# Kernel optimization log

Measured on AMD Instinct MI355X. Metric: run time of the kernel, lower is better.

The kernel has to match this reference:

```python
import jax, jax.numpy as jnp
import numpy as np

K, D = 512, 256
NUM_CLASSES, SHARED_KEYS = 10, 10
B, H, W = 32, 64, 64
TRAINING = True


def setup_inputs() -> dict:
    key = jax.random.key(0)
    k1, k2, k3 = jax.random.split(key, 3)
    z_e_x = jax.random.normal(k1, (B, D, H, W), dtype=jnp.float32)
    labels = jax.random.randint(k2, (B,), 0, NUM_CLASSES)
    # nn.Embedding weight initialized uniform(-1/K, 1/K)
    codebook = jax.random.uniform(k3, (K, D), minval=-1.0 / K, maxval=1.0 / K,
                                  dtype=jnp.float32)
    return {"z_e_x": z_e_x, "codebook": codebook, "labels": labels}


def _irrelevant_regions(labels_flat, k, num_classes, n_shared, training):
    # uniform partition of the first K - n_shared codes over the classes
    uniform = jnp.round(jnp.linspace(-0.5, num_classes - 0.51, k - n_shared))  # [K-Ns]
    irrel = uniform[None, :] != labels_flat[:, None].astype(uniform.dtype)     # [N, K-Ns]
    n = labels_flat.shape[0]
    if training:
        tail = jnp.ones((n, n_shared), dtype=bool)   # TRAIN: shared keys masked out
    else:
        tail = jnp.zeros((n, n_shared), dtype=bool)
    return jnp.concatenate([irrel, tail], axis=1)    # [N, K]


def reference(z_e_x, codebook, labels):
    x = jnp.transpose(z_e_x, (0, 2, 3, 1))           # [B,H,W,D]
    xf = x.reshape(-1, D)                            # [N,D], N=B*H*W
    labels_flat = jnp.repeat(labels, H * W)          # [N]

    irrel = _irrelevant_regions(labels_flat, K, NUM_CLASSES, SHARED_KEYS, TRAINING)

    cb_sqr = jnp.sum(codebook * codebook, axis=1)                      # [K]
    in_sqr = jnp.sum(xf * xf, axis=1, keepdims=True)                   # [N,1]
    distances = in_sqr + cb_sqr[None, :] - 2.0 * (xf @ codebook.T)     # [N,K]
    distances = jnp.where(irrel, jnp.inf, distances)

    idx = jnp.argmin(distances, axis=1)                                # [N]

    codes = codebook[idx].reshape(x.shape)                             # [B,H,W,D]
    # straight-through path (detached codebook in torch)
    z_q = x + jax.lax.stop_gradient(codes - x)
    z_q_x = jnp.transpose(z_q, (0, 3, 1, 2))                           # [B,D,H,W]
    # non-detached codebook lookup path
    z_q_bar = codebook[jax.lax.stop_gradient(idx)].reshape(x.shape)
    z_q_x_bar = jnp.transpose(z_q_bar, (0, 3, 1, 2))                   # [B,D,H,W]
    return (z_q_x, z_q_x_bar)
```

## Files before the change

### kernel.cpp

```cpp
#include <hip/hip_runtime.h>


#define D       256
#define KCODES  512
#define HW      4096
#define BATCH   32
#define NPTS    (BATCH * HW)
#define NWAVES  8
#define WPW     7
#define PTS     128

__constant__ int c_cls_start[11] = {0, 51, 101, 151, 201, 251, 301, 352, 402, 452, 502};

__global__ __launch_bounds__(256) void prep_kernel(const float* __restrict__ cb,
                                                   float* __restrict__ cbT,
                                                   float* __restrict__ cbs) {
    const int k = blockIdx.x;
    const int d = threadIdx.x;
    float v = cb[k * D + d];
    cbT[(size_t)d * KCODES + k] = v;
    __shared__ double red[256];
    red[d] = (double)v * (double)v;
    __syncthreads();
    for (int s = 128; s > 0; s >>= 1) {
        if (d < s) red[d] += red[d + s];
        __syncthreads();
    }
    if (d == 0) cbs[k] = (float)red[0];
}

__global__ __launch_bounds__(512, 8) void vq_kernel(const float* __restrict__ z,
                                                    const int* __restrict__ labels,
                                                    const float* __restrict__ cbT,
                                                    const float* __restrict__ cbs,
                                                    float* __restrict__ out) {
    const int lane = threadIdx.x & 63;
    const int w    = __builtin_amdgcn_readfirstlane(threadIdx.x >> 6);
    const int b    = blockIdx.x >> 5;
    const int hw0  = (blockIdx.x & 31) << 7;
    const int p2   = hw0 | (lane << 1);
    const int lab  = __builtin_amdgcn_readfirstlane(labels[b]);
    const int c0   = c_cls_start[lab];
    const int cnt  = c_cls_start[lab + 1] - c0;
    const int kbase = c0 + w * WPW;
    const int myn   = min(WPW, cnt - w * WPW);

    const float* __restrict__ xp = z + (size_t)b * (D * HW) + p2;

    float acc[WPW][2];
#pragma unroll
    for (int j = 0; j < WPW; ++j) {
        acc[j][0] = 0.0f;
        acc[j][1] = 0.0f;
    }

    double xsq0 = 0.0, xsq1 = 0.0;

    float2 xb[4];
#pragma unroll
    for (int i = 0; i < 4; ++i) xb[i] = *(const float2*)(xp + (size_t)i * HW);

    for (int d = 0; d < D; d += 4) {
        float2 xn[4];
#pragma unroll
        for (int i = 0; i < 4; ++i) {
            int dn = (d + 4 + i) & (D - 1);
            xn[i] = *(const float2*)(xp + (size_t)dn * HW);
        }
#pragma unroll
        for (int i = 0; i < 4; ++i) {
            const float* __restrict__ wd = cbT + (size_t)(d + i) * KCODES + kbase;
            const float2 x = xb[i];
            xsq0 = fma((double)x.x, (double)x.x, xsq0);
            xsq1 = fma((double)x.y, (double)x.y, xsq1);
#pragma unroll
            for (int j = 0; j < WPW; ++j) {
                const float c = wd[j];
                acc[j][0] = fmaf(x.x, c, acc[j][0]);
                acc[j][1] = fmaf(x.y, c, acc[j][1]);
            }
        }
#pragma unroll
        for (int i = 0; i < 4; ++i) xb[i] = xn[i];
    }

    __shared__ float sd[NWAVES][PTS];
    __shared__ int   si[NWAVES][PTS];
#pragma unroll
    for (int p = 0; p < 2; ++p) {
        const float insq = (float)(p == 0 ? xsq0 : xsq1);
        float best = __builtin_inff();
        int bi = kbase;
#pragma unroll
        for (int j = 0; j < WPW; ++j) {
            if (j < myn) {
                float T    = insq + cbs[kbase + j];
                float dist = fmaf(-2.0f, acc[j][p], T);
                if (dist < best) { best = dist; bi = kbase + j; }
            }
        }
        sd[w][(lane << 1) + p] = best;
        si[w][(lane << 1) + p] = bi;
    }
    __syncthreads();

    __shared__ int fidx[PTS];
    if (threadIdx.x < PTS) {
        const int pi = threadIdx.x;
        float fb = sd[0][pi];
        int   fi = si[0][pi];
#pragma unroll
        for (int w2 = 1; w2 < NWAVES; ++w2) {
            float dv = sd[w2][pi];
            if (dv < fb) { fb = dv; fi = si[w2][pi]; }
        }
        fidx[pi] = fi;
    }
    __syncthreads();

    const int f0 = fidx[(lane << 1) + 0];
    const int f1 = fidx[(lane << 1) + 1];

    float* __restrict__ o0 = out + (size_t)b * (D * HW) + p2;
    float* __restrict__ o1 = o0 + (size_t)NPTS * D;
    const int d0 = w * 32;
    const float* __restrict__ cbd = cbT + (size_t)d0 * KCODES;
    for (int d = d0; d < d0 + 32; ++d) {
        float2 v;
        v.x = cbd[f0];
        v.y = cbd[f1];
        *(float2*)(o0 + (size_t)d * HW) = v;
        *(float2*)(o1 + (size_t)d * HW) = v;
        cbd += KCODES;
    }
}

extern "C" void kernel_launch(void* const* d_in, const int* in_sizes, int n_in,
                              void* d_out, int out_size, void* d_ws, size_t ws_size,
                              hipStream_t stream) {
    const float* z      = (const float*)d_in[0];
    const float* cb     = (const float*)d_in[1];
    const int*   labels = (const int*)d_in[2];
    float* out = (float*)d_out;

    float* cbT = (float*)d_ws;
    float* cbs = cbT + (size_t)D * KCODES;

    hipLaunchKernelGGL(prep_kernel, dim3(KCODES), dim3(D), 0, stream, cb, cbT, cbs);
    hipLaunchKernelGGL(vq_kernel, dim3(NPTS / PTS), dim3(512), 0, stream,
                       z, labels, cbT, cbs, out);
}
```

Baseline: 463.6 us.

## Pack per-class codebook slabs and stage activations into LDS via async loads

Codebook entries are repacked into per-class padded slabs of 64 codes, with padding given infinite norm, so each wave handles a uniform 8 codes with no bounds checks. Activation tiles are double-buffered into LDS through global_load_lds, replacing the per-lane register prefetch from global memory. The squared-norm accumulation now runs in only one wave and is shared through LDS. The cost is an extra prep kernel, per-chunk barriers, and more FMA work per wave because of the padding.

```diff
diff --git a/kernel.cpp b/kernel.cpp
--- a/kernel.cpp
+++ b/kernel.cpp
@@ -1,24 +1,47 @@
 #include <hip/hip_runtime.h>
 
 
-#define D       256
-#define KCODES  512
-#define HW      4096
-#define BATCH   32
-#define NPTS    (BATCH * HW)
-#define NWAVES  8
-#define WPW     7
-#define PTS     128
+#define D        256
+#define KCODES   512
+#define HW       4096
+#define BATCH    32
+#define NPTS     (BATCH * HW)
+#define NCLS     10
+#define KPAD     64
+#define NWAVES   8
+#define WPW      8
+#define PTS      128
+#define DC       16
+#define NCHUNK   (D / DC)
 
 __constant__ int c_cls_start[11] = {0, 51, 101, 151, 201, 251, 301, 352, 402, 452, 502};
 
-__global__ __launch_bounds__(256) void prep_kernel(const float* __restrict__ cb,
-                                                   float* __restrict__ cbT,
-                                                   float* __restrict__ cbs) {
+__global__ __launch_bounds__(256) void prep_pack(const float* __restrict__ cb,
+                                                 float* __restrict__ cbP,
+                                                 float* __restrict__ cbsP) {
+    const int cls = blockIdx.x;
+    const int t   = threadIdx.x;
+    const int c0  = c_cls_start[cls];
+    const int cnt = c_cls_start[cls + 1] - c0;
+#pragma unroll 4
+    for (int i = 0; i < (D * KPAD) / 256; ++i) {
+        int idx = i * 256 + t;
+        int d = idx >> 6, j = idx & 63;
+        float v = (j < cnt) ? cb[(size_t)(c0 + j) * D + d] : 0.0f;
+        cbP[((size_t)cls * D + d) * KPAD + j] = v;
+    }
+    if (t < KPAD && t >= cnt) cbsP[cls * KPAD + t] = __builtin_inff();
+}
+
+__global__ __launch_bounds__(256) void prep_sq(const float* __restrict__ cb,
+                                               float* __restrict__ cbsP) {
     const int k = blockIdx.x;
+    if (k >= 502) return;
+    int cls = 0;
+    while (k >= c_cls_start[cls + 1]) ++cls;
+    const int j = k - c_cls_start[cls];
     const int d = threadIdx.x;
-    float v = cb[k * D + d];
-    cbT[(size_t)d * KCODES + k] = v;
+    float v = cb[(size_t)k * D + d];
     __shared__ double red[256];
     red[d] = (double)v * (double)v;
     __syncthreads();
@@ -26,13 +49,13 @@
         if (d < s) red[d] += red[d + s];
         __syncthreads();
     }
-    if (d == 0) cbs[k] = (float)red[0];
+    if (d == 0) cbsP[cls * KPAD + j] = (float)red[0];
 }
 
 __global__ __launch_bounds__(512, 8) void vq_kernel(const float* __restrict__ z,
                                                     const int* __restrict__ labels,
-                                                    const float* __restrict__ cbT,
-                                                    const float* __restrict__ cbs,
+                                                    const float* __restrict__ cbP,
+                                                    const float* __restrict__ cbsP,
                                                     float* __restrict__ out) {
     const int lane = threadIdx.x & 63;
     const int w    = __builtin_amdgcn_readfirstlane(threadIdx.x >> 6);
@@ -40,71 +63,81 @@
     const int hw0  = (blockIdx.x & 31) << 7;
     const int p2   = hw0 | (lane << 1);
     const int lab  = __builtin_amdgcn_readfirstlane(labels[b]);
-    const int c0   = c_cls_start[lab];
-    const int cnt  = c_cls_start[lab + 1] - c0;
-    const int kbase = c0 + w * WPW;
-    const int myn   = min(WPW, cnt - w * WPW);
+    const int jbase = w * WPW;
 
-    const float* __restrict__ xp = z + (size_t)b * (D * HW) + p2;
+    const float* __restrict__ cbw = cbP + (size_t)lab * D * KPAD + jbase;
+    const float* __restrict__ zb  = z + (size_t)b * D * HW + hw0;
+
+    __shared__ float bufX[2][DC][PTS];
+    __shared__ float insq[PTS];
+    __shared__ float sd[NWAVES][PTS];
+    __shared__ int   si[NWAVES][PTS];
+    __shared__ int   fidx[PTS];
+
+    const int srow = 2 * w + (lane >> 5);
+    const int scol = (lane & 31) << 2;
+    auto STAGE = [&](int pb, int c) {
+        const float* g = zb + (size_t)(c * DC + srow) * HW + scol;
+        __builtin_amdgcn_global_load_lds(
+            (const __attribute__((address_space(1))) void*)g,
+            (__attribute__((address_space(3))) void*)&bufX[pb][2 * w][0],
+            16, 0, 0);
+    };
 
     float acc[WPW][2];
 #pragma unroll
-    for (int j = 0; j < WPW; ++j) {
-        acc[j][0] = 0.0f;
-        acc[j][1] = 0.0f;
+    for (int j = 0; j < WPW; ++j) { acc[j][0] = 0.0f; acc[j][1] = 0.0f; }
+    double xsq0 = 0.0, xsq1 = 0.0;
+
+    STAGE(0, 0);
+    __syncthreads();
+
+    for (int c = 0; c < NCHUNK; ++c) {
+        const int pb = c & 1;
+        if (c + 1 < NCHUNK) STAGE(pb ^ 1, c + 1);
+        const float* __restrict__ cbc = cbw + (size_t)(c * DC) * KPAD;
+#pragma unroll
+        for (int dd = 0; dd < DC; ++dd) {
+            const float2 x = *(const float2*)&bufX[pb][dd][lane << 1];
+            const float* __restrict__ cr = cbc + dd * KPAD;
+            if (w == 0) {
+                xsq0 = fma((double)x.x, (double)x.x, xsq0);
+                xsq1 = fma((double)x.y, (double)x.y, xsq1);
+            }
+#pragma unroll
+            for (int j = 0; j < WPW; ++j) {
+                const float cv = cr[j];
+                acc[j][0] = fmaf(x.x, cv, acc[j][0]);
+                acc[j][1] = fmaf(x.y, cv, acc[j][1]);
+            }
+        }
+        __syncthreads();
     }
 
-    double xsq0 = 0.0, xsq1 = 0.0;
-
-    float2 xb[4];
-#pragma unroll
-    for (int i = 0; i < 4; ++i) xb[i] = *(const float2*)(xp + (size_t)i * HW);
-
-    for (int d = 0; d < D; d += 4) {
-        float2 xn[4];
-#pragma unroll
-        for (int i = 0; i < 4; ++i) {
-            int dn = (d + 4 + i) & (D - 1);
-            xn[i] = *(const float2*)(xp + (size_t)dn * HW);
-        }
-#pragma unroll
-        for (int i = 0; i < 4; ++i) {
-            const float* __restrict__ wd = cbT + (size_t)(d + i) * KCODES + kbase;
-            const float2 x = xb[i];
-            xsq0 = fma((double)x.x, (double)x.x, xsq0);
-            xsq1 = fma((double)x.y, (double)x.y, xsq1);
-#pragma unroll
-            for (int j = 0; j < WPW; ++j) {
-                const float c = wd[j];
-                acc[j][0] = fmaf(x.x, c, acc[j][0]);
-                acc[j][1] = fmaf(x.y, c, acc[j][1]);
-            }
-        }
-#pragma unroll
-        for (int i = 0; i < 4; ++i) xb[i] = xn[i];
-    }
-
-    __shared__ float sd[NWAVES][PTS];
-    __shared__ int   si[NWAVES][PTS];
-#pragma unroll
-    for (int p = 0; p < 2; ++p) {
-        const float insq = (float)(p == 0 ? xsq0 : xsq1);
-        float best = __builtin_inff();
-        int bi = kbase;
-#pragma unroll
-        for (int j = 0; j < WPW; ++j) {
-            if (j < myn) {
-                float T    = insq + cbs[kbase + j];
-                float dist = fmaf(-2.0f, acc[j][p], T);
-                if (dist < best) { best = dist; bi = kbase + j; }
-            }
-        }
-        sd[w][(lane << 1) + p] = best;
-        si[w][(lane << 1) + p] = bi;
+    if (w == 0) {
+        float2 iq = make_float2((float)xsq0, (float)xsq1);
+        *(float2*)&insq[lane << 1] = iq;
     }
     __syncthreads();
 
-    __shared__ int fidx[PTS];
+    const float* __restrict__ csq = cbsP + lab * KPAD + jbase;
+    const float2 iq = *(const float2*)&insq[lane << 1];
+    float best0 = __builtin_inff(), best1 = __builtin_inff();
+    int bi0 = jbase, bi1 = jbase;
+#pragma unroll
+    for (int j = 0; j < WPW; ++j) {
+        const float cs = csq[j];
+        float T0 = iq.x + cs;
+        float v0 = fmaf(-2.0f, acc[j][0], T0);
+        if (v0 < best0) { best0 = v0; bi0 = jbase + j; }
+        float T1 = iq.y + cs;
+        float v1 = fmaf(-2.0f, acc[j][1], T1);
+        if (v1 < best1) { best1 = v1; bi1 = jbase + j; }
+    }
+    sd[w][(lane << 1) + 0] = best0;  si[w][(lane << 1) + 0] = bi0;
+    sd[w][(lane << 1) + 1] = best1;  si[w][(lane << 1) + 1] = bi1;
+    __syncthreads();
+
     if (threadIdx.x < PTS) {
         const int pi = threadIdx.x;
         float fb = sd[0][pi];
@@ -118,20 +151,19 @@
     }
     __syncthreads();
 
-    const int f0 = fidx[(lane << 1) + 0];
-    const int f1 = fidx[(lane << 1) + 1];
-
+    const int j0 = fidx[(lane << 1) + 0];
+    const int j1 = fidx[(lane << 1) + 1];
     float* __restrict__ o0 = out + (size_t)b * (D * HW) + p2;
     float* __restrict__ o1 = o0 + (size_t)NPTS * D;
-    const int d0 = w * 32;
-    const float* __restrict__ cbd = cbT + (size_t)d0 * KCODES;
-    for (int d = d0; d < d0 + 32; ++d) {
+    const int d0 = w * (D / NWAVES);
+    const float* __restrict__ crow = cbP + ((size_t)lab * D + d0) * KPAD;
+    for (int d = d0; d < d0 + D / NWAVES; ++d) {
         float2 v;
-        v.x = cbd[f0];
-        v.y = cbd[f1];
+        v.x = crow[j0];
+        v.y = crow[j1];
         *(float2*)(o0 + (size_t)d * HW) = v;
         *(float2*)(o1 + (size_t)d * HW) = v;
-        cbd += KCODES;
+        crow += KPAD;
     }
 }
 
@@ -143,10 +175,11 @@
     const int*   labels = (const int*)d_in[2];
     float* out = (float*)d_out;
 
-    float* cbT = (float*)d_ws;
-    float* cbs = cbT + (size_t)D * KCODES;
+    float* cbP  = (float*)d_ws;
+    float* cbsP = cbP + (size_t)NCLS * D * KPAD;
 
-    hipLaunchKernelGGL(prep_kernel, dim3(KCODES), dim3(D), 0, stream, cb, cbT, cbs);
+    hipLaunchKernelGGL(prep_pack, dim3(NCLS), dim3(256), 0, stream, cb, cbP, cbsP);
+    hipLaunchKernelGGL(prep_sq, dim3(KCODES), dim3(256), 0, stream, cb, cbsP);
     hipLaunchKernelGGL(vq_kernel, dim3(NPTS / PTS), dim3(512), 0, stream,
-                       z, labels, cbT, cbs, out);
+                       z, labels, cbP, cbsP, out);
 }
```

Result: slower. 613.5 us (+32.3%).
